# Kernel optimization log

Hardware: AMD Instinct MI355X
Metric: run time of the kernel (lower is better)

The kernel has to match this reference:

```python
import jax, jax.numpy as jnp
import numpy as np

SQRT2 = float(np.sqrt(2.0))


def setup_inputs() -> dict:
    key = jax.random.key(0)
    ks = jax.random.split(key, 6)
    B, Cin, Cout, S, H, W = 8, 64, 64, 512, 256, 256
    return {
        "x": jax.random.normal(ks[0], (B, Cin, H, W), dtype=jnp.float32),
        "w": jax.random.normal(ks[1], (B, S), dtype=jnp.float32),
        "noise": jax.random.normal(ks[2], (B, 1, H, W), dtype=jnp.float32),
        "lin_w": jax.random.normal(ks[3], (Cin, S), dtype=jnp.float32),
        "lin_b": jnp.ones((Cin,), dtype=jnp.float32),
        "conv_w": jax.random.normal(ks[4], (Cout, Cin, 3, 3), dtype=jnp.float32),
        "noise_weight": jax.random.normal(ks[5], (), dtype=jnp.float32) * 0.1,
        "act_bias": jnp.zeros((Cout,), dtype=jnp.float32),
    }


def reference(x, w, noise, lin_w, lin_b, conv_w, noise_weight, act_bias):
    B, Cin, H, W = x.shape
    Cout = conv_w.shape[0]
    # EqualLinear style transform: weight scaled by 1/sqrt(fan_in), bias init 1
    lin_scale = 1.0 / np.sqrt(lin_w.shape[1])
    y = w @ (lin_w * lin_scale).T + lin_b  # [B, Cin] per-sample channel scales
    # Modulate: equalized conv scale * per-sample style
    conv_scale = 1.0 / np.sqrt(Cin * 3 * 3)
    wm = conv_w[None] * conv_scale * y[:, None, :, None, None]  # [B,Cout,Cin,3,3]
    # Demodulate
    demod = jax.lax.rsqrt(jnp.sum(wm * wm, axis=(2, 3, 4)) + 1e-8)  # [B,Cout]
    wm = wm * demod[:, :, None, None, None]
    # Grouped conv trick: batch folded into channels, groups = B
    xg = x.reshape(1, B * Cin, H, W)
    wg = wm.reshape(B * Cout, Cin, 3, 3)
    out = jax.lax.conv_general_dilated(
        xg, wg, window_strides=(1, 1), padding=[(1, 1), (1, 1)],
        dimension_numbers=("NCHW", "OIHW", "NCHW"), feature_group_count=B,
    ).reshape(B, Cout, H, W)
    # Noise injection + equalized leaky relu (bias, slope 0.2, gain sqrt(2))
    out = out + noise_weight * noise
    z = out + act_bias[None, :, None, None]
    return jax.nn.leaky_relu(z, negative_slope=0.2) * SQRT2
```

## Files before the change

kernel.cpp:

```cpp
#include <hip/hip_runtime.h>
#include <hip/hip_bf16.h>

#define Bn 8
#define Cc 64
#define Hh 256
#define Ww 256
#define Ss 512

typedef __attribute__((ext_vector_type(8))) short short8;
typedef __attribute__((ext_vector_type(4))) float floatx4;

__device__ __forceinline__ unsigned f2bf_bits(float f) {
    unsigned u = __float_as_uint(f);
    return (u + 0x7FFFu + ((u >> 16) & 1u)) >> 16;
}

__device__ __forceinline__ unsigned pack_bf2(float lo, float hi) {
    __hip_bfloat162 p = __float22bfloat162_rn(make_float2(lo, hi));
    union { __hip_bfloat162 h; unsigned u; } cv;
    cv.h = p;
    return cv.u;
}

__global__ void k_style(const float* __restrict__ w,
                        const float* __restrict__ lin_w,
                        const float* __restrict__ lin_b,
                        float* __restrict__ y) {
    int bc = blockIdx.x;
    int b = bc >> 6, c = bc & 63;
    int lane = threadIdx.x;
    float acc = 0.f;
#pragma unroll
    for (int i = 0; i < Ss / 64; ++i) {
        int s = i * 64 + lane;
        acc += w[b * Ss + s] * lin_w[c * Ss + s];
    }
#pragma unroll
    for (int off = 32; off >= 1; off >>= 1) acc += __shfl_xor(acc, off, 64);
    if (lane == 0)
        y[bc] = acc * 0.04419417382415922f  + lin_b[c];
}

__global__ void k_weights(const float* __restrict__ conv_w,
                          const float* __restrict__ y,
                          short* __restrict__ wt) {
    int bco = blockIdx.x;
    int b = bco >> 6, co = bco & 63;
    int ci = threadIdx.x;
    const float conv_scale = 1.0f / 24.0f;
    float yv = y[b * Cc + ci] * conv_scale;
    float wv[9];
    float ss = 0.f;
#pragma unroll
    for (int k = 0; k < 9; ++k) {
        float v = conv_w[(co * Cc + ci) * 9 + k] * yv;
        wv[k] = v;
        ss += v * v;
    }
#pragma unroll
    for (int off = 32; off >= 1; off >>= 1) ss += __shfl_xor(ss, off, 64);
    float demod = rsqrtf(ss + 1e-8f);
    int s = ci >> 5, cl = ci & 31;
#pragma unroll
    for (int t = 0; t < 9; ++t)
        wt[(((b * 2 + s) * 9 + t) * Cc + co) * 32 + cl] =
            (short)f2bf_bits(wv[t] * demod);
}

__global__ __launch_bounds__(256, 3) void k_mfma(
    const float* __restrict__ x,
    const short* __restrict__ wt,
    const float* __restrict__ noise,
    const float* __restrict__ nw_p,
    const float* __restrict__ act_bias,
    float* __restrict__ out) {
    __shared__ short xs[6 * 66 * 40];

    const int tid = threadIdx.x;
    const int wave = tid >> 6, lane = tid & 63;
    const int l15 = lane & 15, quad = lane >> 4;

    const int bid = blockIdx.x;
    const int swz = (bid & 7) * 256 + (bid >> 3);
    const int b = swz >> 8;
    const int rem = swz & 255;
    const int w0 = (rem & 3) * 64, h0 = (rem >> 2) * 4;

    const int cg = tid & 15;
    const int rc0 = tid >> 4;

    floatx4 acc[4][4];
#pragma unroll
    for (int mt = 0; mt < 4; ++mt)
#pragma unroll
        for (int nt = 0; nt < 4; ++nt)
            acc[mt][nt] = (floatx4){0.f, 0.f, 0.f, 0.f};

    for (int s = 0; s < 2; ++s) {
        if (s) __syncthreads();

        {
            int r = rc0, cp = 0;
            if (r >= 6) { r -= 6; cp = 1; }
            if (r >= 6) { r -= 6; cp = 2; }
            const int c = 1 + cg * 4;
#pragma unroll
            for (int it = 0; it < 6; ++it) {
                const int gh = h0 + r - 1;
                float4 lo4 = make_float4(0.f, 0.f, 0.f, 0.f);
                float4 hi4 = make_float4(0.f, 0.f, 0.f, 0.f);
                if ((unsigned)gh < (unsigned)Hh) {
                    const float* xp = x +
                        (((size_t)(b * Cc + s * 32 + cp * 2)) << 16) +
                        gh * Ww + (w0 + cg * 4);
                    lo4 = *(const float4*)xp;
                    hi4 = *(const float4*)(xp + Hh * Ww);
                }
                const float lov[4] = {lo4.x, lo4.y, lo4.z, lo4.w};
                const float hiv[4] = {hi4.x, hi4.y, hi4.z, hi4.w};
                unsigned* dst = (unsigned*)xs + (r * 66 + c) * 20 + cp;
#pragma unroll
                for (int j = 0; j < 4; ++j)
                    dst[j * 20] = pack_bf2(lov[j], hiv[j]);
                r += 4; cp += 2;
                if (r >= 6) { r -= 6; ++cp; }
            }
        }
        if (tid < 192) {
            const int side = tid & 1;
            const int rc = tid >> 1;
            const int hr = rc % 6, hcp = rc / 6;
            const int gh = h0 + hr - 1;
            const int gw = side ? (w0 + 64) : (w0 - 1);
            float lo = 0.f, hi = 0.f;
            if ((unsigned)gh < (unsigned)Hh && (unsigned)gw < (unsigned)Ww) {
                const float* xp = x +
                    (((size_t)(b * Cc + s * 32 + hcp * 2)) << 16) +
                    gh * Ww + gw;
                lo = xp[0];
                hi = xp[Hh * Ww];
            }
            ((unsigned*)xs)[(hr * 66 + (side ? 65 : 0)) * 20 + hcp] =
                pack_bf2(lo, hi);
        }
        __syncthreads();

        const short* wbase = wt + (size_t)((b * 2 + s) * 9) * Cc * 32;
#pragma unroll
        for (int t = 0; t < 9; ++t) {
            const int dr = t / 3, dc = t % 3;
            short8 bfr[4];
#pragma unroll
            for (int nt = 0; nt < 4; ++nt)
                bfr[nt] = *(const short8*)(xs +
                    ((wave + dr) * 66 + (nt * 16 + l15 + dc)) * 40 + quad * 8);
            short8 afr[4];
#pragma unroll
            for (int mt = 0; mt < 4; ++mt)
                afr[mt] = *(const short8*)(wbase +
                    ((t * Cc + mt * 16 + l15) * 32 + quad * 8));
#pragma unroll
            for (int mt = 0; mt < 4; ++mt)
#pragma unroll
                for (int nt = 0; nt < 4; ++nt)
                    acc[mt][nt] = __builtin_amdgcn_mfma_f32_16x16x32_bf16(
                        afr[mt], bfr[nt], acc[mt][nt], 0, 0, 0);
        }
    }

    const int h = h0 + wave;
    const float nw = nw_p[0];
    float nz[4];
#pragma unroll
    for (int nt = 0; nt < 4; ++nt)
        nz[nt] = nw * noise[((size_t)b * Hh + h) * Ww + w0 + nt * 16 + l15];
#pragma unroll
    for (int mt = 0; mt < 4; ++mt) {
#pragma unroll
        for (int reg = 0; reg < 4; ++reg) {
            int co = mt * 16 + quad * 4 + reg;
            float bias = act_bias[co];
#pragma unroll
            for (int nt = 0; nt < 4; ++nt) {
                float v = acc[mt][nt][reg] + nz[nt] + bias;
                v = (v > 0.f ? v : 0.2f * v) * 1.41421356237f;
                out[(((size_t)(b * Cc + co)) * Hh + h) * Ww + w0 + nt * 16 + l15] = v;
            }
        }
    }
}

extern "C" void kernel_launch(void* const* d_in, const int* in_sizes, int n_in,
                              void* d_out, int out_size, void* d_ws, size_t ws_size,
                              hipStream_t stream) {
    const float* x        = (const float*)d_in[0];
    const float* w        = (const float*)d_in[1];
    const float* noise    = (const float*)d_in[2];
    const float* lin_w    = (const float*)d_in[3];
    const float* lin_b    = (const float*)d_in[4];
    const float* conv_w   = (const float*)d_in[5];
    const float* nw_p     = (const float*)d_in[6];
    const float* act_bias = (const float*)d_in[7];

    float* y  = (float*)d_ws;
    short* wtb = (short*)((char*)d_ws + 4096);

    k_style<<<Bn * Cc, 64, 0, stream>>>(w, lin_w, lin_b, y);
    k_weights<<<Bn * Cc, 64, 0, stream>>>(conv_w, y, wtb);

    k_mfma<<<dim3(2048, 1, 1), 256, 0, stream>>>(x, wtb, noise, nw_p, act_bias,
                                                 (float*)d_out);
}
```

Measured before the change: 321.2 us.

## Split output channels across 8 waves and pad LDS cells to 42 shorts

Doubles the block to 512 threads. Each pair of waves now shares one output row, with each wave computing half of the 64 output channels, so each wave holds half as many accumulators. The input staging loop is remapped so the extra threads share the load, running 3 iterations instead of 6. The LDS cell stride goes from 40 to 42 shorts and the row stride is padded, aiming to reduce bank conflicts on the B-fragment reads. The risks are that the 128-bit LDS reads are no longer 16-byte aligned, and that launch bounds of (512,4) tighten the register budget and may cause spills.

```diff
diff --git a/kernel.cpp b/kernel.cpp
--- a/kernel.cpp
+++ b/kernel.cpp
@@ -6,6 +6,9 @@
 #define Hh 256
 #define Ww 256
 #define Ss 512
+
+#define LCELL 42
+#define LROW  2778
 
 typedef __attribute__((ext_vector_type(8))) short short8;
 typedef __attribute__((ext_vector_type(4))) float floatx4;
@@ -67,18 +70,20 @@
             (short)f2bf_bits(wv[t] * demod);
 }
 
-__global__ __launch_bounds__(256, 3) void k_mfma(
+__global__ __launch_bounds__(512, 4) void k_mfma(
     const float* __restrict__ x,
     const short* __restrict__ wt,
     const float* __restrict__ noise,
     const float* __restrict__ nw_p,
     const float* __restrict__ act_bias,
     float* __restrict__ out) {
-    __shared__ short xs[6 * 66 * 40];
+    __shared__ short xs[6 * LROW];
 
     const int tid = threadIdx.x;
     const int wave = tid >> 6, lane = tid & 63;
     const int l15 = lane & 15, quad = lane >> 4;
+    const int wr = wave >> 1;
+    const int wm = wave & 1;
 
     const int bid = blockIdx.x;
     const int swz = (bid & 7) * 256 + (bid >> 3);
@@ -89,12 +94,12 @@
     const int cg = tid & 15;
     const int rc0 = tid >> 4;
 
-    floatx4 acc[4][4];
-#pragma unroll
-    for (int mt = 0; mt < 4; ++mt)
+    floatx4 acc[2][4];
+#pragma unroll
+    for (int mi = 0; mi < 2; ++mi)
 #pragma unroll
         for (int nt = 0; nt < 4; ++nt)
-            acc[mt][nt] = (floatx4){0.f, 0.f, 0.f, 0.f};
+            acc[mi][nt] = (floatx4){0.f, 0.f, 0.f, 0.f};
 
     for (int s = 0; s < 2; ++s) {
         if (s) __syncthreads();
@@ -103,9 +108,12 @@
             int r = rc0, cp = 0;
             if (r >= 6) { r -= 6; cp = 1; }
             if (r >= 6) { r -= 6; cp = 2; }
+            if (r >= 6) { r -= 6; cp = 3; }
+            if (r >= 6) { r -= 6; cp = 4; }
+            if (r >= 6) { r -= 6; cp = 5; }
             const int c = 1 + cg * 4;
 #pragma unroll
-            for (int it = 0; it < 6; ++it) {
+            for (int it = 0; it < 3; ++it) {
                 const int gh = h0 + r - 1;
                 float4 lo4 = make_float4(0.f, 0.f, 0.f, 0.f);
                 float4 hi4 = make_float4(0.f, 0.f, 0.f, 0.f);
@@ -118,11 +126,11 @@
                 }
                 const float lov[4] = {lo4.x, lo4.y, lo4.z, lo4.w};
                 const float hiv[4] = {hi4.x, hi4.y, hi4.z, hi4.w};
-                unsigned* dst = (unsigned*)xs + (r * 66 + c) * 20 + cp;
+                unsigned* dst = (unsigned*)xs + r * 1389 + c * 21 + cp;
 #pragma unroll
                 for (int j = 0; j < 4; ++j)
-                    dst[j * 20] = pack_bf2(lov[j], hiv[j]);
-                r += 4; cp += 2;
+                    dst[j * 21] = pack_bf2(lov[j], hiv[j]);
+                r += 2; cp += 5;
                 if (r >= 6) { r -= 6; ++cp; }
             }
         }
@@ -140,7 +148,7 @@
                 lo = xp[0];
                 hi = xp[Hh * Ww];
             }
-            ((unsigned*)xs)[(hr * 66 + (side ? 65 : 0)) * 20 + hcp] =
+            ((unsigned*)xs)[hr * 1389 + (side ? 65 : 0) * 21 + hcp] =
                 pack_bf2(lo, hi);
         }
         __syncthreads();
@@ -153,36 +161,36 @@
 #pragma unroll
             for (int nt = 0; nt < 4; ++nt)
                 bfr[nt] = *(const short8*)(xs +
-                    ((wave + dr) * 66 + (nt * 16 + l15 + dc)) * 40 + quad * 8);
-            short8 afr[4];
-#pragma unroll
-            for (int mt = 0; mt < 4; ++mt)
-                afr[mt] = *(const short8*)(wbase +
-                    ((t * Cc + mt * 16 + l15) * 32 + quad * 8));
-#pragma unroll
-            for (int mt = 0; mt < 4; ++mt)
+                    (wr + dr) * LROW + (nt * 16 + l15 + dc) * LCELL + quad * 8);
+            short8 afr[2];
+#pragma unroll
+            for (int mi = 0; mi < 2; ++mi)
+                afr[mi] = *(const short8*)(wbase +
+                    ((t * Cc + (wm * 2 + mi) * 16 + l15) * 32 + quad * 8));
+#pragma unroll
+            for (int mi = 0; mi < 2; ++mi)
 #pragma unroll
                 for (int nt = 0; nt < 4; ++nt)
-                    acc[mt][nt] = __builtin_amdgcn_mfma_f32_16x16x32_bf16(
-                        afr[mt], bfr[nt], acc[mt][nt], 0, 0, 0);
-        }
-    }
-
-    const int h = h0 + wave;
+                    acc[mi][nt] = __builtin_amdgcn_mfma_f32_16x16x32_bf16(
+                        afr[mi], bfr[nt], acc[mi][nt], 0, 0, 0);
+        }
+    }
+
+    const int h = h0 + wr;
     const float nw = nw_p[0];
     float nz[4];
 #pragma unroll
     for (int nt = 0; nt < 4; ++nt)
         nz[nt] = nw * noise[((size_t)b * Hh + h) * Ww + w0 + nt * 16 + l15];
 #pragma unroll
-    for (int mt = 0; mt < 4; ++mt) {
+    for (int mi = 0; mi < 2; ++mi) {
 #pragma unroll
         for (int reg = 0; reg < 4; ++reg) {
-            int co = mt * 16 + quad * 4 + reg;
+            int co = (wm * 2 + mi) * 16 + quad * 4 + reg;
             float bias = act_bias[co];
 #pragma unroll
             for (int nt = 0; nt < 4; ++nt) {
-                float v = acc[mt][nt][reg] + nz[nt] + bias;
+                float v = acc[mi][nt][reg] + nz[nt] + bias;
                 v = (v > 0.f ? v : 0.2f * v) * 1.41421356237f;
                 out[(((size_t)(b * Cc + co)) * Hh + h) * Ww + w0 + nt * 16 + l15] = v;
             }
@@ -208,6 +216,6 @@
     k_style<<<Bn * Cc, 64, 0, stream>>>(w, lin_w, lin_b, y);
     k_weights<<<Bn * Cc, 64, 0, stream>>>(conv_w, y, wtb);
 
-    k_mfma<<<dim3(2048, 1, 1), 256, 0, stream>>>(x, wtb, noise, nw_p, act_bias,
+    k_mfma<<<dim3(2048, 1, 1), 512, 0, stream>>>(x, wtb, noise, nw_p, act_bias,
                                                  (float*)d_out);
 }
```

Measured after the change: 298.8 us. 1.07x faster.

## Split conv tile across 8 waves and XOR-swizzle LDS input layout

Applied to the files above, without the earlier changes.

The MFMA conv kernel now uses 512 threads per block. Each of the 8 waves computes one output row and half of the 64 columns, so each wave holds half as many accumulators. The shared-memory input tile gets an odd row pad and an XOR swizzle on the channel-pair slot, aimed at removing LDS bank conflicts on the fragment loads. In exchange, each wave reloads the full weight fragments for half the MFMA work, and the tighter launch bounds (512 threads, 4 blocks) cap registers and may cause spills.

```diff
diff --git a/kernel.cpp b/kernel.cpp
--- a/kernel.cpp
+++ b/kernel.cpp
@@ -6,6 +6,10 @@
 #define Hh 256
 #define Ww 256
 #define Ss 512
+
+#define LROW_U  1321
+#define LROW_S  2642
+#define LCELL_S 40
 
 typedef __attribute__((ext_vector_type(8))) short short8;
 typedef __attribute__((ext_vector_type(4))) float floatx4;
@@ -67,18 +71,20 @@
             (short)f2bf_bits(wv[t] * demod);
 }
 
-__global__ __launch_bounds__(256, 3) void k_mfma(
+__global__ __launch_bounds__(512, 4) void k_mfma(
     const float* __restrict__ x,
     const short* __restrict__ wt,
     const float* __restrict__ noise,
     const float* __restrict__ nw_p,
     const float* __restrict__ act_bias,
     float* __restrict__ out) {
-    __shared__ short xs[6 * 66 * 40];
+    __shared__ short xs[6 * LROW_S];
 
     const int tid = threadIdx.x;
     const int wave = tid >> 6, lane = tid & 63;
     const int l15 = lane & 15, quad = lane >> 4;
+    const int wr = wave >> 1;
+    const int n0 = (wave & 1) * 2;
 
     const int bid = blockIdx.x;
     const int swz = (bid & 7) * 256 + (bid >> 3);
@@ -89,12 +95,14 @@
     const int cg = tid & 15;
     const int rc0 = tid >> 4;
 
-    floatx4 acc[4][4];
+    floatx4 acc[4][2];
 #pragma unroll
     for (int mt = 0; mt < 4; ++mt)
 #pragma unroll
-        for (int nt = 0; nt < 4; ++nt)
-            acc[mt][nt] = (floatx4){0.f, 0.f, 0.f, 0.f};
+        for (int ni = 0; ni < 2; ++ni)
+            acc[mt][ni] = (floatx4){0.f, 0.f, 0.f, 0.f};
+
+    unsigned* const xsu = (unsigned*)xs;
 
     for (int s = 0; s < 2; ++s) {
         if (s) __syncthreads();
@@ -103,9 +111,12 @@
             int r = rc0, cp = 0;
             if (r >= 6) { r -= 6; cp = 1; }
             if (r >= 6) { r -= 6; cp = 2; }
-            const int c = 1 + cg * 4;
-#pragma unroll
-            for (int it = 0; it < 6; ++it) {
+            if (r >= 6) { r -= 6; cp = 3; }
+            if (r >= 6) { r -= 6; cp = 4; }
+            if (r >= 6) { r -= 6; cp = 5; }
+            const int cbase = 1 + cg * 4;
+#pragma unroll
+            for (int it = 0; it < 3; ++it) {
                 const int gh = h0 + r - 1;
                 float4 lo4 = make_float4(0.f, 0.f, 0.f, 0.f);
                 float4 hi4 = make_float4(0.f, 0.f, 0.f, 0.f);
@@ -118,11 +129,14 @@
                 }
                 const float lov[4] = {lo4.x, lo4.y, lo4.z, lo4.w};
                 const float hiv[4] = {hi4.x, hi4.y, hi4.z, hi4.w};
-                unsigned* dst = (unsigned*)xs + (r * 66 + c) * 20 + cp;
-#pragma unroll
-                for (int j = 0; j < 4; ++j)
-                    dst[j * 20] = pack_bf2(lov[j], hiv[j]);
-                r += 4; cp += 2;
+#pragma unroll
+                for (int j = 0; j < 4; ++j) {
+                    const int c = cbase + j;
+                    xsu[r * LROW_U + c * 20 +
+                        (cp ^ ((((unsigned)c >> 3) & 3) << 2))] =
+                        pack_bf2(lov[j], hiv[j]);
+                }
+                r += 2; cp += 5;
                 if (r >= 6) { r -= 6; ++cp; }
             }
         }
@@ -140,8 +154,7 @@
                 lo = xp[0];
                 hi = xp[Hh * Ww];
             }
-            ((unsigned*)xs)[(hr * 66 + (side ? 65 : 0)) * 20 + hcp] =
-                pack_bf2(lo, hi);
+            xsu[hr * LROW_U + (side ? 65 : 0) * 20 + hcp] = pack_bf2(lo, hi);
         }
         __syncthreads();
 
@@ -149,11 +162,13 @@
 #pragma unroll
         for (int t = 0; t < 9; ++t) {
             const int dr = t / 3, dc = t % 3;
-            short8 bfr[4];
-#pragma unroll
-            for (int nt = 0; nt < 4; ++nt)
-                bfr[nt] = *(const short8*)(xs +
-                    ((wave + dr) * 66 + (nt * 16 + l15 + dc)) * 40 + quad * 8);
+            short8 bfr[2];
+#pragma unroll
+            for (int ni = 0; ni < 2; ++ni) {
+                const int c = (n0 + ni) * 16 + l15 + dc;
+                bfr[ni] = *(const short8*)(xs + (wr + dr) * LROW_S + c * LCELL_S +
+                    ((quad * 8) ^ ((((unsigned)c >> 3) & 3) << 3)));
+            }
             short8 afr[4];
 #pragma unroll
             for (int mt = 0; mt < 4; ++mt)
@@ -162,18 +177,18 @@
 #pragma unroll
             for (int mt = 0; mt < 4; ++mt)
 #pragma unroll
-                for (int nt = 0; nt < 4; ++nt)
-                    acc[mt][nt] = __builtin_amdgcn_mfma_f32_16x16x32_bf16(
-                        afr[mt], bfr[nt], acc[mt][nt], 0, 0, 0);
-        }
-    }
-
-    const int h = h0 + wave;
+                for (int ni = 0; ni < 2; ++ni)
+                    acc[mt][ni] = __builtin_amdgcn_mfma_f32_16x16x32_bf16(
+                        afr[mt], bfr[ni], acc[mt][ni], 0, 0, 0);
+        }
+    }
+
+    const int h = h0 + wr;
     const float nw = nw_p[0];
-    float nz[4];
-#pragma unroll
-    for (int nt = 0; nt < 4; ++nt)
-        nz[nt] = nw * noise[((size_t)b * Hh + h) * Ww + w0 + nt * 16 + l15];
+    float nz[2];
+#pragma unroll
+    for (int ni = 0; ni < 2; ++ni)
+        nz[ni] = nw * noise[((size_t)b * Hh + h) * Ww + w0 + (n0 + ni) * 16 + l15];
 #pragma unroll
     for (int mt = 0; mt < 4; ++mt) {
 #pragma unroll
@@ -181,10 +196,11 @@
             int co = mt * 16 + quad * 4 + reg;
             float bias = act_bias[co];
 #pragma unroll
-            for (int nt = 0; nt < 4; ++nt) {
-                float v = acc[mt][nt][reg] + nz[nt] + bias;
+            for (int ni = 0; ni < 2; ++ni) {
+                float v = acc[mt][ni][reg] + nz[ni] + bias;
                 v = (v > 0.f ? v : 0.2f * v) * 1.41421356237f;
-                out[(((size_t)(b * Cc + co)) * Hh + h) * Ww + w0 + nt * 16 + l15] = v;
+                out[(((size_t)(b * Cc + co)) * Hh + h) * Ww +
+                    w0 + (n0 + ni) * 16 + l15] = v;
             }
         }
     }
@@ -208,6 +224,6 @@
     k_style<<<Bn * Cc, 64, 0, stream>>>(w, lin_w, lin_b, y);
     k_weights<<<Bn * Cc, 64, 0, stream>>>(conv_w, y, wtb);
 
-    k_mfma<<<dim3(2048, 1, 1), 256, 0, stream>>>(x, wtb, noise, nw_p, act_bias,
+    k_mfma<<<dim3(2048, 1, 1), 512, 0, stream>>>(x, wtb, noise, nw_p, act_bias,
                                                  (float*)d_out);
 }
```

Result: slower. 343.0 us (+6.8%).
